# Kernel tuning notes

Measured on AMD Instinct MI355X. Metric: run time of the kernel, lower is better.

## Reference

```python
import jax, jax.numpy as jnp
import numpy as np

N = 16384   # num nodes
E = 524288  # num edges (avg degree 32)
C = 128     # in_channels == hidden_channels (residual requires equality)


def setup_inputs() -> dict:
    key = jax.random.key(0)
    ks = jax.random.split(key, 16)
    s = 1.0 / np.sqrt(C)  # glorot-ish scale
    return {
        "x": jax.random.normal(ks[0], (N, C), dtype=jnp.float32),
        "edge_index": jax.random.randint(ks[1], (2, E), 0, N, dtype=jnp.int32),
        "edge_attr": jax.random.normal(ks[2], (E, 8), dtype=jnp.float32),
        # GATConv 1 params
        "W1": jax.random.normal(ks[3], (C, C), dtype=jnp.float32) * s,
        "a_src1": jax.random.normal(ks[4], (C,), dtype=jnp.float32) * s,
        "a_dst1": jax.random.normal(ks[5], (C,), dtype=jnp.float32) * s,
        "b1": jnp.zeros((C,), dtype=jnp.float32),
        # GATConv 2 params
        "W2": jax.random.normal(ks[6], (C, C), dtype=jnp.float32) * s,
        "a_src2": jax.random.normal(ks[7], (C,), dtype=jnp.float32) * s,
        "a_dst2": jax.random.normal(ks[8], (C,), dtype=jnp.float32) * s,
        "b2": jnp.zeros((C,), dtype=jnp.float32),
        # TemporalAttention params
        "att_weight": jax.random.normal(ks[9], (C, C), dtype=jnp.float32) * s,
        "att_bias": jnp.zeros((C,), dtype=jnp.float32),
        # LayerNorm params
        "ln_gamma": jnp.ones((C,), dtype=jnp.float32),
        "ln_beta": jnp.zeros((C,), dtype=jnp.float32),
    }


def _gat_conv(x, edge_index, W, a_src, a_dst, b):
    """PyG GATConv, heads=1, negative_slope=0.2, add_self_loops=True.
    Edge (j -> i): src = edge_index[0], dst = edge_index[1]; softmax over dst."""
    n = x.shape[0]
    xw = x @ W                                   # [N, C]
    loops = jnp.arange(n, dtype=edge_index.dtype)
    src = jnp.concatenate([edge_index[0], loops])  # [E+N]
    dst = jnp.concatenate([edge_index[1], loops])
    alpha_src = xw @ a_src                       # [N]
    alpha_dst = xw @ a_dst                       # [N]
    e = jax.nn.leaky_relu(alpha_src[src] + alpha_dst[dst], negative_slope=0.2)
    # numerically stable segment softmax over destination nodes
    e_max = jax.ops.segment_max(e, dst, num_segments=n)
    p = jnp.exp(e - e_max[dst])
    denom = jax.ops.segment_sum(p, dst, num_segments=n)
    alpha = p / denom[dst]                       # [E+N]
    out = jax.ops.segment_sum(alpha[:, None] * xw[src], dst, num_segments=n)
    return out + b


def reference(x, edge_index, edge_attr, W1, a_src1, a_dst1, b1,
              W2, a_src2, a_dst2, b2, att_weight, att_bias, ln_gamma, ln_beta):
    # edge_attr is accepted but unused: GATConv was built without edge_dim,
    # so PyG ignores it in the attention computation.
    h = jax.nn.relu(_gat_conv(x, edge_index, W1, a_src1, a_dst1, b1))
    # dropout p=0.2 is identity in eval mode
    h = _gat_conv(h, edge_index, W2, a_src2, a_dst2, b2)

    # TemporalAttention over the (batch=1, N, C) view -> dense NxN attention
    q = h @ att_weight                            # [N, C]
    scores = (q @ h.T) / jnp.sqrt(jnp.float32(h.shape[-1]))  # [N, N]
    attn = jax.nn.softmax(scores, axis=-1)
    h = attn @ h + att_bias                       # [N, C]

    h = h + x                                     # residual
    mu = jnp.mean(h, axis=-1, keepdims=True)
    var = jnp.var(h, axis=-1, keepdims=True)
    h = (h - mu) / jnp.sqrt(var + 1e-5) * ln_gamma + ln_beta
    return h
```

## Files before the change

kernel.cpp:

```cpp
#include <hip/hip_runtime.h>

#define CC 128

typedef __attribute__((ext_vector_type(8))) short bf16x8;
typedef __attribute__((ext_vector_type(16))) float f32x16;

static __device__ __forceinline__ float lrelu(float v){ return v > 0.f ? v : 0.2f*v; }
static __device__ __forceinline__ unsigned short f2bf(float f){
  unsigned u = __float_as_uint(f);
  unsigned r = (u + 0x7fffu + ((u >> 16) & 1u)) >> 16;
  return (unsigned short)r;
}
static __device__ __forceinline__ float bf2f(unsigned short s){
  return __uint_as_float(((unsigned)s) << 16);
}
static __device__ __forceinline__ unsigned cvtpk(float lo, float hi){
  unsigned r;
  asm("v_cvt_pk_bf16_f32 %0, %1, %2" : "=v"(r) : "v"(lo), "v"(hi));
  return r;
}

#define QSCALE (0.08838834764831845f * 1.4426950408889634f)
#define L2E 1.4426950408889634f

#if defined(__has_builtin)
#if __has_builtin(__builtin_amdgcn_global_load_lds)
#define HAVE_GLL 1
#endif
#endif

#ifdef HAVE_GLL
static __device__ __forceinline__ void gload_lds16(const uint4* g, uint4* l){
  __builtin_amdgcn_global_load_lds(
      (const __attribute__((address_space(1))) unsigned int*)(const void*)g,
      (__attribute__((address_space(3))) unsigned int*)(void*)l, 16, 0, 0);
}
#endif

__global__ __launch_bounds__(256) void pack_w3(const float* __restrict__ W1,
                                               const float* __restrict__ W2,
                                               const float* __restrict__ Wa,
                                               unsigned short* __restrict__ img){
  int gid = blockIdx.x*256 + threadIdx.x;
  int m = gid >> 11, u = gid & 2047;
  const float* W = (m==0) ? W1 : (m==1) ? W2 : Wa;
  int k = u >> 8, ct = (u >> 6) & 3, l = u & 63;
  int h = l >> 5, c = ct*32 + (l & 31);
  int k0 = k*16 + h*8;
  float f[8];
  #pragma unroll
  for (int j=0;j<8;j++) f[j] = W[(k0+j)*CC + c];
  uint4 o;
  o.x = cvtpk(f[0],f[1]); o.y = cvtpk(f[2],f[3]);
  o.z = cvtpk(f[4],f[5]); o.w = cvtpk(f[6],f[7]);
  *(uint4*)&img[((size_t)m*2048 + u)*8] = o;
}

template<bool ABF16, int OMODE>
__global__ __launch_bounds__(256) void gemm_mfma(const void* __restrict__ Av,
                                                 const uint4* __restrict__ Wimg,
                                                 unsigned short* __restrict__ out){
  __shared__ uint4 WS[2048];
  const int tid = threadIdx.x, lane = tid & 63, w = tid >> 6;
  const int h = lane >> 5, l31 = lane & 31;
  const long r0 = (long)blockIdx.x * 64;
#ifdef HAVE_GLL
  #pragma unroll
  for (int i=0;i<8;i++){ int u = i*256 + w*64; gload_lds16(Wimg + u + lane, &WS[u]); }
#else
  #pragma unroll
  for (int i=0;i<8;i++){ int u = i*256 + tid; WS[u] = Wimg[u]; }
#endif
  const int rt = w & 1, ct0 = (w >> 1) * 2;
  const long arow = (r0 + rt*32 + l31)*CC + h*8;
  f32x16 acc0 = {}, acc1 = {};
  __syncthreads();
  #pragma unroll
  for (int k=0;k<8;k++){
    bf16x8 afr;
    if (ABF16){
      afr = *(const bf16x8*)&((const unsigned short*)Av)[arow + k*16];
    } else {
      const float* ap = (const float*)Av + arow + k*16;
      float4 a0 = *(const float4*)ap;
      float4 a1 = *(const float4*)(ap+4);
      uint4 av;
      av.x = cvtpk(a0.x,a0.y); av.y = cvtpk(a0.z,a0.w);
      av.z = cvtpk(a1.x,a1.y); av.w = cvtpk(a1.z,a1.w);
      __builtin_memcpy(&afr, &av, 16);
    }
    bf16x8 b0 = *(const bf16x8*)&WS[(k*4+ct0  )*64 + lane];
    bf16x8 b1 = *(const bf16x8*)&WS[(k*4+ct0+1)*64 + lane];
    acc0 = __builtin_amdgcn_mfma_f32_32x32x16_bf16(afr, b0, acc0, 0,0,0);
    acc1 = __builtin_amdgcn_mfma_f32_32x32x16_bf16(afr, b1, acc1, 0,0,0);
  }
  #pragma unroll
  for (int r=0;r<16;r++){
    long row = r0 + rt*32 + (r&3) + 8*(r>>2) + 4*h;
    float s0 = (OMODE==1) ? acc0[r]*QSCALE : acc0[r];
    float s1 = (OMODE==1) ? acc1[r]*QSCALE : acc1[r];
    out[row*CC + ct0*32 + l31]     = f2bf(s0);
    out[row*CC + (ct0+1)*32 + l31] = f2bf(s1);
  }
}

__global__ __launch_bounds__(256) void rowdot2b(const unsigned short* __restrict__ X,
                                                const float* __restrict__ a1,
                                                const float* __restrict__ a2,
                                                float* __restrict__ as_, float* __restrict__ ad_){
  const int lane = threadIdx.x & 63;
  const long row = (long)blockIdx.x*4 + (threadIdx.x >> 6);
  unsigned u = *(const unsigned*)&X[row*CC + lane*2];
  float v0 = bf2f((unsigned short)(u & 0xffffu));
  float v1 = bf2f((unsigned short)(u >> 16));
  float2 w1 = ((const float2*)a1)[lane];
  float2 w2 = ((const float2*)a2)[lane];
  float s1 = v0*w1.x + v1*w1.y;
  float s2 = v0*w2.x + v1*w2.y;
  #pragma unroll
  for (int off=32; off; off>>=1){
    s1 += __shfl_xor(s1, off);
    s2 += __shfl_xor(s2, off);
  }
  if (lane==0){ as_[row]=s1; ad_[row]=s2; }
}

__global__ void zero_int(int* __restrict__ p, int n){
  int i = blockIdx.x*256 + threadIdx.x;
  if (i < n) p[i] = 0;
}
__global__ void csr_hist(const int* __restrict__ ei, int* __restrict__ deg, int E){
  int e = blockIdx.x*256 + threadIdx.x;
  if (e < E) atomicAdd(&deg[ei[E + e]], 1);
}
__global__ __launch_bounds__(256) void csr_scan(const int* __restrict__ deg,
                                                int* __restrict__ rowptr,
                                                int* __restrict__ cursor, int N){
  __shared__ int part[257];
  const int t = threadIdx.x;
  const int per = N / 256;
  const int base = t*per;
  int s = 0;
  for (int j=0;j<per;j++) s += deg[base+j];
  part[t+1] = s;
  if (t==0) part[0] = 0;
  __syncthreads();
  if (t==0){
    for (int i=1;i<=256;i++) part[i] += part[i-1];
  }
  __syncthreads();
  int run = part[t];
  for (int j=0;j<per;j++){
    rowptr[base+j] = run;
    cursor[base+j] = run;
    run += deg[base+j];
  }
  if (t==255) rowptr[N] = run;
}
__global__ void csr_fill(const int* __restrict__ ei, int* __restrict__ cursor,
                         int* __restrict__ csrc, int E){
  int e = blockIdx.x*256 + threadIdx.x;
  if (e < E){
    int d = ei[E + e];
    int slot = atomicAdd(&cursor[d], 1);
    csrc[slot] = ei[e];
  }
}

template<bool RELUOUT>
__global__ __launch_bounds__(256) void gat_gather(
    const int* __restrict__ rowptr, const int* __restrict__ csrc,
    const float* __restrict__ as_, const float* __restrict__ ad_,
    const unsigned short* __restrict__ X, const float* __restrict__ b,
    unsigned short* __restrict__ O, int N){
  const int lane = threadIdx.x & 63;
  const int half = lane >> 5, l32 = lane & 31;
  const int dst = blockIdx.x*4 + (threadIdx.x >> 6);
  const float adv = ad_[dst];
  float m = lrelu(as_[dst] + adv);
  float l = 1.f;
  float acc0=0.f, acc1=0.f, acc2=0.f, acc3=0.f;
  if (half == 0){
    ushort4 v = *(const ushort4*)&X[(size_t)dst*CC + l32*4];
    acc0 = bf2f(v.x); acc1 = bf2f(v.y); acc2 = bf2f(v.z); acc3 = bf2f(v.w);
  }
  const int kb = rowptr[dst];
  const int deg = rowptr[dst+1] - kb;
  for (int c0 = 0; c0 < deg; c0 += 64){
    const int nv = min(64, deg - c0);
    int src = dst; float e = -3.0e38f;
    if (lane < nv){
      src = csrc[kb + c0 + lane];
      e = lrelu(as_[src] + adv);
    }
    float cm = e;
    #pragma unroll
    for (int off=32; off; off>>=1) cm = fmaxf(cm, __shfl_xor(cm, off));
    if (cm > m){
      float fr = __builtin_amdgcn_exp2f((m - cm)*L2E);
      l *= fr; acc0 *= fr; acc1 *= fr; acc2 *= fr; acc3 *= fr;
      m = cm;
    }
    float p = __builtin_amdgcn_exp2f((e - m)*L2E);
    float cs = p;
    #pragma unroll
    for (int off=32; off; off>>=1) cs += __shfl_xor(cs, off);
    l += cs;
    for (int j = 0; j < nv; j += 2){
      float w0 = __shfl(p, j);
      float w1 = __shfl(p, (j+1)&63);
      w1 = (j+1 < nv) ? w1 : 0.f;
      int s0 = __shfl(src, j);
      int s1 = __shfl(src, (j+1)&63);
      float wgt = half ? w1 : w0;
      int s = half ? s1 : s0;
      ushort4 v = *(const ushort4*)&X[(size_t)s*CC + l32*4];
      acc0 += wgt*bf2f(v.x); acc1 += wgt*bf2f(v.y);
      acc2 += wgt*bf2f(v.z); acc3 += wgt*bf2f(v.w);
    }
  }
  acc0 += __shfl_xor(acc0, 32);
  acc1 += __shfl_xor(acc1, 32);
  acc2 += __shfl_xor(acc2, 32);
  acc3 += __shfl_xor(acc3, 32);
  if (half == 0){
    float inv = 1.f / l;
    float4 bb = *(const float4*)&b[l32*4];
    float r0 = acc0*inv + bb.x, r1 = acc1*inv + bb.y;
    float r2 = acc2*inv + bb.z, r3 = acc3*inv + bb.w;
    if (RELUOUT){
      r0=fmaxf(r0,0.f); r1=fmaxf(r1,0.f); r2=fmaxf(r2,0.f); r3=fmaxf(r3,0.f);
    }
    uint2 o; o.x = cvtpk(r0,r1); o.y = cvtpk(r2,r3);
    *(uint2*)&O[(size_t)dst*CC + l32*4] = o;
  }
}

template<int NKT>
__global__ __launch_bounds__(256) void convert_pack(const unsigned short* __restrict__ h,
                                                    uint4* __restrict__ IMG, int N){
  const int KVB = NKT*32;
  int idx = blockIdx.x*256 + threadIdx.x;
  int tile = idx / (NKT*1024);
  int u = idx - tile*(NKT*1024);
  int l = u & 63, hh = l >> 5, l31 = l & 31;
  if (u < NKT*512){
    int kt = u >> 9, ks = (u >> 6) & 7;
    int key = tile*KVB + kt*32 + l31;
    IMG[idx] = *(const uint4*)&h[(size_t)key*CC + ks*16 + hh*8];
  } else {
    int v = u - NKT*512;
    int ks = (v >> 6) & (2*NKT - 1);
    int ct = v >> (NKT==1 ? 7 : 8);
    int c = ct*32 + l31;
    int key0 = tile*KVB + ks*16 + hh*8;
    unsigned short o[8];
    #pragma unroll
    for (int j=0;j<8;j++) o[j] = h[(size_t)(key0+j)*CC + c];
    IMG[idx] = *(uint4*)o;
  }
}

template<int NKT, int NQT>
__global__ __launch_bounds__(256,2) void attn_mfma(
    const unsigned short* __restrict__ Qb, const uint4* __restrict__ IMG,
    unsigned short* __restrict__ opW, float* __restrict__ ml, int N, int nsplit){
  const int TILE4 = NKT*1024;
  __shared__ uint4 SH[2*NKT*1024];

  const int tid = threadIdx.x;
  const int lane = tid & 63, w = tid >> 6;
  const int h = lane >> 5, q31 = lane & 31;
  const int flat = blockIdx.x;
  const int split = flat % nsplit;
  const int qb0 = (flat / nsplit) * (128*NQT);
  const int KVB = NKT*32;
  const int ntt = N / KVB;
  const int tb = (ntt*split)/nsplit, te = (ntt*(split+1))/nsplit;

  int qrow[NQT];
  bf16x8 qf[NQT][8];
  #pragma unroll
  for (int qt=0; qt<NQT; qt++){
    qrow[qt] = qb0 + w*(32*NQT) + qt*32 + q31;
    #pragma unroll
    for (int ks=0; ks<8; ks++)
      qf[qt][ks] = *(const bf16x8*)&Qb[(size_t)qrow[qt]*CC + ks*16 + h*8];
  }

  f32x16 zero16 = {};
  f32x16 acc_o[4][NQT];
  #pragma unroll
  for (int ct=0; ct<4; ct++)
    #pragma unroll
    for (int qt=0; qt<NQT; qt++) acc_o[ct][qt] = zero16;
  float m_[NQT], l_[NQT];
  #pragma unroll
  for (int qt=0; qt<NQT; qt++){ m_[qt] = -3.0e38f; l_[qt] = 0.f; }

  int cur = 0;
  {
    const uint4* src = IMG + (size_t)tb*TILE4;
#ifdef HAVE_GLL
    #pragma unroll
    for (int i=0;i<NKT*4;i++){ int u = i*256 + w*64; gload_lds16(src + u + lane, &SH[u]); }
#else
    #pragma unroll
    for (int i=0;i<NKT*4;i++){ int u = i*256 + tid; SH[u] = src[u]; }
#endif
  }

  for (int t=tb; t<te; t++){
    __syncthreads();
    if (t+1 < te){
      const uint4* src = IMG + (size_t)(t+1)*TILE4;
      uint4* dst = &SH[(cur^1)*TILE4];
#ifdef HAVE_GLL
      #pragma unroll
      for (int i=0;i<NKT*4;i++){ int u = i*256 + w*64; gload_lds16(src + u + lane, dst + u); }
#else
      #pragma unroll
      for (int i=0;i<NKT*4;i++){ int u = i*256 + tid; dst[u] = src[u]; }
#endif
    }
    const uint4* B = &SH[cur*TILE4];

    f32x16 accs[NKT][NQT];
    #pragma unroll
    for (int kt=0; kt<NKT; kt++){
      #pragma unroll
      for (int qt=0; qt<NQT; qt++) accs[kt][qt] = zero16;
      __builtin_amdgcn_s_setprio(1);
      #pragma unroll
      for (int ks=0; ks<8; ks++){
        bf16x8 hf = *(const bf16x8*)&B[(kt*8+ks)*64 + lane];
        #pragma unroll
        for (int qt=0; qt<NQT; qt++)
          accs[kt][qt] = __builtin_amdgcn_mfma_f32_32x32x16_bf16(hf, qf[qt][ks], accs[kt][qt], 0,0,0);
      }
      __builtin_amdgcn_s_setprio(0);
    }

    float tm[NQT];
    #pragma unroll
    for (int qt=0; qt<NQT; qt++){
      float tmax[16];
      #pragma unroll
      for (int r=0;r<16;r++){
        float v = accs[0][qt][r];
        if (NKT == 2) v = fmaxf(v, accs[1][qt][r]);
        tmax[r] = v;
      }
      #pragma unroll
      for (int s=8; s; s>>=1)
        #pragma unroll
        for (int r=0;r<s;r++) tmax[r] = fmaxf(tmax[r], tmax[r+s]);
      tm[qt] = fmaxf(tmax[0], __shfl_xor(tmax[0], 32));
    }
    bool ok = true;
    #pragma unroll
    for (int qt=0; qt<NQT; qt++) ok &= (tm[qt] <= m_[qt] + 11.0f);
    if (!__all(ok)){
      #pragma unroll
      for (int qt=0; qt<NQT; qt++){
        float mn = fmaxf(m_[qt], tm[qt]);
        float fr = __builtin_amdgcn_exp2f(m_[qt] - mn);
        m_[qt] = mn; l_[qt] *= fr;
        #pragma unroll
        for (int ct=0; ct<4; ct++)
          #pragma unroll
          for (int r=0;r<16;r++) acc_o[ct][qt][r] *= fr;
      }
    }
    unsigned pk[NQT][NKT][8];
    #pragma unroll
    for (int qt=0; qt<NQT; qt++){
      float psum[16];
      #pragma unroll
      for (int kt=0; kt<NKT; kt++)
        #pragma unroll
        for (int r=0;r<16;r++)
          accs[kt][qt][r] = __builtin_amdgcn_exp2f(accs[kt][qt][r] - m_[qt]);
      #pragma unroll
      for (int r=0;r<16;r++){
        float v = accs[0][qt][r];
        if (NKT == 2) v += accs[1][qt][r];
        psum[r] = v;
      }
      #pragma unroll
      for (int s=8; s; s>>=1)
        #pragma unroll
        for (int r=0;r<s;r++) psum[r] += psum[r+s];
      l_[qt] += psum[0] + __shfl_xor(psum[0], 32);
      #pragma unroll
      for (int kt=0; kt<NKT; kt++)
        #pragma unroll
        for (int wd=0; wd<8; wd++)
          pk[qt][kt][wd] = cvtpk(accs[kt][qt][2*wd], accs[kt][qt][2*wd+1]);
    }

    #pragma unroll
    for (int ks=0; ks<2*NKT; ks++){
      const int kt = ks >> 1, W = (ks & 1)*4;
      bf16x8 pfrag[NQT];
      #pragma unroll
      for (int qt=0; qt<NQT; qt++){
        unsigned w0o = pk[qt][kt][W+0], w1o = pk[qt][kt][W+1];
        unsigned w2o = pk[qt][kt][W+2], w3o = pk[qt][kt][W+3];
        unsigned va = h ? w0o : w2o;
        unsigned vb = h ? w1o : w3o;
        unsigned fa = (unsigned)__shfl_xor((int)va, 32);
        unsigned fb = (unsigned)__shfl_xor((int)vb, 32);
        uint4 fw;
        fw.x = h ? fa : w0o;
        fw.y = h ? fb : w1o;
        fw.z = h ? w2o : fa;
        fw.w = h ? w3o : fb;
        __builtin_memcpy(&pfrag[qt], &fw, 16);
      }
      __builtin_amdgcn_s_setprio(1);
      #pragma unroll
      for (int ct=0; ct<4; ct++){
        bf16x8 hf = *(const bf16x8*)&B[NKT*512 + (ct*2*NKT+ks)*64 + lane];
        #pragma unroll
        for (int qt=0; qt<NQT; qt++)
          acc_o[ct][qt] = __builtin_amdgcn_mfma_f32_32x32x16_bf16(hf, pfrag[qt], acc_o[ct][qt], 0,0,0);
      }
      __builtin_amdgcn_s_setprio(0);
    }
    cur ^= 1;
  }

  #pragma unroll
  for (int qt=0; qt<NQT; qt++){
    float inv = 1.f / l_[qt];
    unsigned apk[4][8];
    #pragma unroll
    for (int ct=0; ct<4; ct++)
      #pragma unroll
      for (int wd=0; wd<8; wd++)
        apk[ct][wd] = cvtpk(acc_o[ct][qt][2*wd]*inv, acc_o[ct][qt][2*wd+1]*inv);

    unsigned short* orow = opW + (size_t)split*N*CC + (size_t)qrow[qt]*CC + h*64;
    #pragma unroll
    for (int cp=0; cp<2; cp++){
      #pragma unroll
      for (int jp=0; jp<4; jp++){
        int wd0 = 2*jp, wd1 = 2*jp+1;
        unsigned a0 = apk[cp][wd0],   a1 = apk[cp][wd1];
        unsigned b0 = apk[cp+2][wd0], b1 = apk[cp+2][wd1];
        unsigned v0 = h ? a0 : b0;
        unsigned v1 = h ? a1 : b1;
        unsigned f0 = (unsigned)__shfl_xor((int)v0, 32);
        unsigned f1 = (unsigned)__shfl_xor((int)v1, 32);
        unsigned o0 = h ? b0 : a0;
        unsigned o1 = h ? b1 : a1;
        uint4 st;
        st.x = h ? f0 : o0;
        st.y = h ? f1 : o1;
        st.z = h ? o0 : f0;
        st.w = h ? o1 : f1;
        *(uint4*)&orow[cp*32 + jp*8] = st;
      }
    }
    if (lane < 32)
      ((float2*)ml)[(size_t)split*N + qrow[qt]] = make_float2(m_[qt], l_[qt]);
  }
}

template<int NS>
__global__ __launch_bounds__(256) void merge_ln(
    const unsigned short* __restrict__ opW, const float* __restrict__ ml,
    const float* __restrict__ x, const float* __restrict__ ab,
    const float* __restrict__ gam, const float* __restrict__ bet,
    float* __restrict__ out, int N){
  const int lane = threadIdx.x & 63;
  const long row = (long)blockIdx.x*4 + (threadIdx.x >> 6);
  float mm[NS], ll[NS];
  float M = -3.0e38f;
  #pragma unroll
  for (int i=0;i<NS;i++){
    float2 v = ((const float2*)ml)[(size_t)i*N + row];
    mm[i]=v.x; ll[i]=v.y;
    M = fmaxf(M, v.x);
  }
  float den = 0.f;
  float wgt[NS];
  #pragma unroll
  for (int i=0;i<NS;i++){ wgt[i] = exp2f(mm[i]-M)*ll[i]; den += wgt[i]; }
  float invd = 1.f/den;
  float o0 = 0.f, o1 = 0.f;
  #pragma unroll
  for (int i=0;i<NS;i++){
    unsigned u = *(const unsigned*)&opW[((size_t)i*N + row)*CC + lane*2];
    float c = wgt[i]*invd;
    o0 += c * bf2f((unsigned short)(u & 0xffffu));
    o1 += c * bf2f((unsigned short)(u >> 16));
  }
  float2 xb = ((const float2*)(x + row*CC))[lane];
  float2 bb = ((const float2*)ab)[lane];
  float a0 = o0 + bb.x + xb.x;
  float a1 = o1 + bb.y + xb.y;
  float s = a0 + a1, ss = a0*a0 + a1*a1;
  #pragma unroll
  for (int off=32; off; off>>=1){ s += __shfl_xor(s,off); ss += __shfl_xor(ss,off); }
  float mu  = s * (1.f/128.f);
  float var = ss * (1.f/128.f) - mu*mu;
  float rstd = rsqrtf(var + 1e-5f);
  float2 gg = ((const float2*)gam)[lane];
  float2 b2 = ((const float2*)bet)[lane];
  float2 r;
  r.x = (a0 - mu)*rstd*gg.x + b2.x;
  r.y = (a1 - mu)*rstd*gg.y + b2.y;
  ((float2*)(out + row*CC))[lane] = r;
}

extern "C" void kernel_launch(void* const* d_in, const int* in_sizes, int n_in,
                              void* d_out, int out_size, void* d_ws, size_t ws_size,
                              hipStream_t stream) {
  const float* x   = (const float*)d_in[0];
  const int*   ei  = (const int*)d_in[1];
  const float* W1  = (const float*)d_in[3];
  const float* a_s1= (const float*)d_in[4];
  const float* a_d1= (const float*)d_in[5];
  const float* b1  = (const float*)d_in[6];
  const float* W2  = (const float*)d_in[7];
  const float* a_s2= (const float*)d_in[8];
  const float* a_d2= (const float*)d_in[9];
  const float* b2  = (const float*)d_in[10];
  const float* Wa  = (const float*)d_in[11];
  const float* ab  = (const float*)d_in[12];
  const float* g   = (const float*)d_in[13];
  const float* be  = (const float*)d_in[14];
  float* out = (float*)d_out;

  const int N = in_sizes[0] / CC;
  const int E = in_sizes[1] / 2;
  const size_t MB = 1024*1024;
  const size_t KB = 1024;

  char* base = (char*)d_ws;
  uint4* IMG  = (uint4*)(base);
  unsigned short* xwb = (unsigned short*)(base + 8*MB);
  unsigned short* hW  = (unsigned short*)(base + 12*MB);
  int* csrc   = (int*)(base + 16*MB);
  int* rowptr = (int*)(base + 18*MB);
  int* cursor = (int*)(base + 18*MB + 128*KB);
  int* deg    = (int*)(base + 18*MB + 256*KB);
  float* as_  = (float*)(base + 18*MB + 384*KB);
  float* ad_  = (float*)(base + 18*MB + 512*KB);
  unsigned short* Wimg = (unsigned short*)(base + 19*MB);
  unsigned short* opW  = (unsigned short*)(base + 8*MB);
  unsigned short* QbD  = (unsigned short*)d_out;

  const uint4* W1i = (const uint4*)(Wimg);
  const uint4* W2i = (const uint4*)(Wimg + 2048*8);
  const uint4* Wai = (const uint4*)(Wimg + 2*2048*8);

  const bool big = (ws_size >= 41*MB);
  const int ns = big ? 8 : 4;
  float* ml = (float*)(base + 8*MB + (size_t)ns*4*MB);

  dim3 B(256);

  pack_w3<<<24, B, 0, stream>>>(W1, W2, Wa, Wimg);
  zero_int<<<(N+255)/256, B, 0, stream>>>(deg, N);
  csr_hist<<<(E+255)/256, B, 0, stream>>>(ei, deg, E);
  csr_scan<<<1, B, 0, stream>>>(deg, rowptr, cursor, N);
  csr_fill<<<(E+255)/256, B, 0, stream>>>(ei, cursor, csrc, E);

  gemm_mfma<false,0><<<N/64, B, 0, stream>>>(x, W1i, xwb);
  rowdot2b<<<N/4, B, 0, stream>>>(xwb, a_s1, a_d1, as_, ad_);
  gat_gather<true><<<N/4, B, 0, stream>>>(rowptr, csrc, as_, ad_, xwb, b1, hW, N);

  gemm_mfma<true,0><<<N/64, B, 0, stream>>>(hW, W2i, xwb);
  rowdot2b<<<N/4, B, 0, stream>>>(xwb, a_s2, a_d2, as_, ad_);
  gat_gather<false><<<N/4, B, 0, stream>>>(rowptr, csrc, as_, ad_, xwb, b2, hW, N);

  gemm_mfma<true,1><<<N/64, B, 0, stream>>>(hW, Wai, QbD);
  if (big){
    convert_pack<1><<<(N*32)/256, B, 0, stream>>>(hW, IMG, N);
    attn_mfma<1,2><<<(N/256)*8, B, 0, stream>>>(QbD, IMG, opW, ml, N, 8);
    merge_ln<8><<<N/4, B, 0, stream>>>(opW, ml, x, ab, g, be, out, N);
  } else {
    convert_pack<2><<<(N*32)/256, B, 0, stream>>>(hW, IMG, N);
    attn_mfma<2,1><<<(N/128)*4, B, 0, stream>>>(QbD, IMG, opW, ml, N, 4);
    merge_ln<4><<<N/4, B, 0, stream>>>(opW, ml, x, ab, g, be, out, N);
  }
}
```

Measured before the change: 321.0 us.

## Widen GAT gather to 16-byte loads and add 16-way attention key split

The GAT gather kernel now processes four edges per wave iteration, with 16 lanes per edge each loading 8 bf16 values via 16-byte loads, instead of two edges with 8-byte loads. It reduces partial sums across the four groups with two shuffle stages. The aim is more memory-level parallelism in the irregular neighbour gathers. Separately, when the workspace is large enough the dense attention is split across 16 key segments instead of 8, giving more blocks at the cost of a heavier merge step. The bf16 unpacking is also simplified to mask and shift on the packed word.

After: 323.8 us. Within noise of the previous version (+0.9%).

```diff
diff --git a/kernel.cpp b/kernel.cpp
--- a/kernel.cpp
+++ b/kernel.cpp
@@ -13,6 +13,12 @@
 }
 static __device__ __forceinline__ float bf2f(unsigned short s){
   return __uint_as_float(((unsigned)s) << 16);
+}
+static __device__ __forceinline__ float bf2f_lo(unsigned u){
+  return __uint_as_float(u << 16);
+}
+static __device__ __forceinline__ float bf2f_hi(unsigned u){
+  return __uint_as_float(u & 0xffff0000u);
 }
 static __device__ __forceinline__ unsigned cvtpk(float lo, float hi){
   unsigned r;
@@ -111,8 +117,8 @@
   const int lane = threadIdx.x & 63;
   const long row = (long)blockIdx.x*4 + (threadIdx.x >> 6);
   unsigned u = *(const unsigned*)&X[row*CC + lane*2];
-  float v0 = bf2f((unsigned short)(u & 0xffffu));
-  float v1 = bf2f((unsigned short)(u >> 16));
+  float v0 = bf2f_lo(u);
+  float v1 = bf2f_hi(u);
   float2 w1 = ((const float2*)a1)[lane];
   float2 w2 = ((const float2*)a2)[lane];
   float s1 = v0*w1.x + v1*w1.y;
@@ -174,15 +180,18 @@
     const unsigned short* __restrict__ X, const float* __restrict__ b,
     unsigned short* __restrict__ O, int N){
   const int lane = threadIdx.x & 63;
-  const int half = lane >> 5, l32 = lane & 31;
+  const int g = lane >> 4, l16 = lane & 15;
   const int dst = blockIdx.x*4 + (threadIdx.x >> 6);
   const float adv = ad_[dst];
   float m = lrelu(as_[dst] + adv);
   float l = 1.f;
-  float acc0=0.f, acc1=0.f, acc2=0.f, acc3=0.f;
-  if (half == 0){
-    ushort4 v = *(const ushort4*)&X[(size_t)dst*CC + l32*4];
-    acc0 = bf2f(v.x); acc1 = bf2f(v.y); acc2 = bf2f(v.z); acc3 = bf2f(v.w);
+  float acc[8] = {0.f,0.f,0.f,0.f,0.f,0.f,0.f,0.f};
+  if (g == 0){
+    uint4 v = *(const uint4*)&X[(size_t)dst*CC + l16*8];
+    acc[0]=bf2f_lo(v.x); acc[1]=bf2f_hi(v.x);
+    acc[2]=bf2f_lo(v.y); acc[3]=bf2f_hi(v.y);
+    acc[4]=bf2f_lo(v.z); acc[5]=bf2f_hi(v.z);
+    acc[6]=bf2f_lo(v.w); acc[7]=bf2f_hi(v.w);
   }
   const int kb = rowptr[dst];
   const int deg = rowptr[dst+1] - kb;
@@ -198,7 +207,9 @@
     for (int off=32; off; off>>=1) cm = fmaxf(cm, __shfl_xor(cm, off));
     if (cm > m){
       float fr = __builtin_amdgcn_exp2f((m - cm)*L2E);
-      l *= fr; acc0 *= fr; acc1 *= fr; acc2 *= fr; acc3 *= fr;
+      l *= fr;
+      #pragma unroll
+      for (int k=0;k<8;k++) acc[k] *= fr;
       m = cm;
     }
     float p = __builtin_amdgcn_exp2f((e - m)*L2E);
@@ -206,33 +217,38 @@
     #pragma unroll
     for (int off=32; off; off>>=1) cs += __shfl_xor(cs, off);
     l += cs;
-    for (int j = 0; j < nv; j += 2){
-      float w0 = __shfl(p, j);
-      float w1 = __shfl(p, (j+1)&63);
-      w1 = (j+1 < nv) ? w1 : 0.f;
-      int s0 = __shfl(src, j);
-      int s1 = __shfl(src, (j+1)&63);
-      float wgt = half ? w1 : w0;
-      int s = half ? s1 : s0;
-      ushort4 v = *(const ushort4*)&X[(size_t)s*CC + l32*4];
-      acc0 += wgt*bf2f(v.x); acc1 += wgt*bf2f(v.y);
-      acc2 += wgt*bf2f(v.z); acc3 += wgt*bf2f(v.w);
-    }
-  }
-  acc0 += __shfl_xor(acc0, 32);
-  acc1 += __shfl_xor(acc1, 32);
-  acc2 += __shfl_xor(acc2, 32);
-  acc3 += __shfl_xor(acc3, 32);
-  if (half == 0){
+    for (int j = 0; j < nv; j += 4){
+      int idx = j + g;
+      float w_e = __shfl(p, idx);
+      int   s_e = __shfl(src, idx);
+      uint4 v = *(const uint4*)&X[(size_t)s_e*CC + l16*8];
+      acc[0] += w_e*bf2f_lo(v.x); acc[1] += w_e*bf2f_hi(v.x);
+      acc[2] += w_e*bf2f_lo(v.y); acc[3] += w_e*bf2f_hi(v.y);
+      acc[4] += w_e*bf2f_lo(v.z); acc[5] += w_e*bf2f_hi(v.z);
+      acc[6] += w_e*bf2f_lo(v.w); acc[7] += w_e*bf2f_hi(v.w);
+    }
+  }
+  #pragma unroll
+  for (int k=0;k<8;k++){
+    acc[k] += __shfl_xor(acc[k], 16);
+    acc[k] += __shfl_xor(acc[k], 32);
+  }
+  if (g == 0){
     float inv = 1.f / l;
-    float4 bb = *(const float4*)&b[l32*4];
-    float r0 = acc0*inv + bb.x, r1 = acc1*inv + bb.y;
-    float r2 = acc2*inv + bb.z, r3 = acc3*inv + bb.w;
+    float4 b0 = *(const float4*)&b[l16*8];
+    float4 b1 = *(const float4*)&b[l16*8 + 4];
+    float r0 = acc[0]*inv + b0.x, r1 = acc[1]*inv + b0.y;
+    float r2 = acc[2]*inv + b0.z, r3 = acc[3]*inv + b0.w;
+    float r4 = acc[4]*inv + b1.x, r5 = acc[5]*inv + b1.y;
+    float r6 = acc[6]*inv + b1.z, r7 = acc[7]*inv + b1.w;
     if (RELUOUT){
       r0=fmaxf(r0,0.f); r1=fmaxf(r1,0.f); r2=fmaxf(r2,0.f); r3=fmaxf(r3,0.f);
-    }
-    uint2 o; o.x = cvtpk(r0,r1); o.y = cvtpk(r2,r3);
-    *(uint2*)&O[(size_t)dst*CC + l32*4] = o;
+      r4=fmaxf(r4,0.f); r5=fmaxf(r5,0.f); r6=fmaxf(r6,0.f); r7=fmaxf(r7,0.f);
+    }
+    uint4 o;
+    o.x = cvtpk(r0,r1); o.y = cvtpk(r2,r3);
+    o.z = cvtpk(r4,r5); o.w = cvtpk(r6,r7);
+    *(uint4*)&O[(size_t)dst*CC + l16*8] = o;
   }
 }
 
@@ -494,8 +510,8 @@
   for (int i=0;i<NS;i++){
     unsigned u = *(const unsigned*)&opW[((size_t)i*N + row)*CC + lane*2];
     float c = wgt[i]*invd;
-    o0 += c * bf2f((unsigned short)(u & 0xffffu));
-    o1 += c * bf2f((unsigned short)(u >> 16));
+    o0 += c * bf2f_lo(u);
+    o1 += c * bf2f_hi(u);
   }
   float2 xb = ((const float2*)(x + row*CC))[lane];
   float2 bb = ((const float2*)ab)[lane];
@@ -557,8 +573,10 @@
   const uint4* W2i = (const uint4*)(Wimg + 2048*8);
   const uint4* Wai = (const uint4*)(Wimg + 2*2048*8);
 
-  const bool big = (ws_size >= 41*MB);
-  const int ns = big ? 8 : 4;
+  int ns;
+  if (ws_size >= 74*MB)      ns = 16;
+  else if (ws_size >= 41*MB) ns = 8;
+  else                       ns = 4;
   float* ml = (float*)(base + 8*MB + (size_t)ns*4*MB);
 
   dim3 B(256);
@@ -578,10 +596,13 @@
   gat_gather<false><<<N/4, B, 0, stream>>>(rowptr, csrc, as_, ad_, xwb, b2, hW, N);
 
   gemm_mfma<true,1><<<N/64, B, 0, stream>>>(hW, Wai, QbD);
-  if (big){
+  if (ns >= 8){
     convert_pack<1><<<(N*32)/256, B, 0, stream>>>(hW, IMG, N);
-    attn_mfma<1,2><<<(N/256)*8, B, 0, stream>>>(QbD, IMG, opW, ml, N, 8);
-    merge_ln<8><<<N/4, B, 0, stream>>>(opW, ml, x, ab, g, be, out, N);
+    attn_mfma<1,2><<<(N/256)*ns, B, 0, stream>>>(QbD, IMG, opW, ml, N, ns);
+    if (ns == 16)
+      merge_ln<16><<<N/4, B, 0, stream>>>(opW, ml, x, ab, g, be, out, N);
+    else
+      merge_ln<8><<<N/4, B, 0, stream>>>(opW, ml, x, ab, g, be, out, N);
   } else {
     convert_pack<2><<<(N*32)/256, B, 0, stream>>>(hW, IMG, N);
     attn_mfma<2,1><<<(N/128)*4, B, 0, stream>>>(QbD, IMG, opW, ml, N, 4);
```
